# Performance work log

Hardware: AMD Instinct MI355X
Metric: run time of the kernel (lower is better)

The kernel has to match this reference:

```python
import jax, jax.numpy as jnp
import numpy as np

D_MODEL = 256
D_INNER = 512   # expand=2
D_STATE = 16
D_CONV = 4
DT_RANK = 16    # ceil(d_model/16)


def _mamba(x, in_w, conv_w, conv_b, xproj_w, dt_w, dt_b, A_log, Dskip, out_w):
    # x: (B, T, d_model)
    B, T, _ = x.shape
    xz = x @ in_w.T                       # (B, T, 2*d_inner)
    u, z = jnp.split(xz, 2, axis=-1)
    # depthwise causal conv1d over time
    uc = u.transpose(0, 2, 1)             # (B, d_inner, T)
    up = jnp.pad(uc, ((0, 0), (0, 0), (D_CONV - 1, 0)))
    conv = conv_b[None, :, None]
    for k in range(D_CONV):               # tiny fixed loop over taps
        conv = conv + conv_w[None, :, k, None] * up[:, :, k:k + T]
    u = jax.nn.silu(conv).transpose(0, 2, 1)   # (B, T, d_inner)
    # input-dependent SSM params
    x_dbl = u @ xproj_w.T                 # (B, T, dt_rank + 2*d_state)
    dt, Bm, Cm = jnp.split(x_dbl, [DT_RANK, DT_RANK + D_STATE], axis=-1)
    delta = jax.nn.softplus(dt @ dt_w.T + dt_b)   # (B, T, d_inner)
    A = -jnp.exp(A_log)                   # (d_inner, d_state)
    dA = jnp.exp(jnp.einsum('btd,dn->btdn', delta, A))
    dBu = jnp.einsum('btd,btn,btd->btdn', delta, Bm, u)

    def step(h, inp):
        dA_t, dBu_t, C_t = inp
        h = dA_t * h + dBu_t              # (B, d_inner, d_state)
        y = jnp.einsum('bdn,bn->bd', h, C_t)
        return h, y

    h0 = jnp.zeros((B, D_INNER, D_STATE), x.dtype)
    _, ys = jax.lax.scan(step, h0, (dA.transpose(1, 0, 2, 3),
                                    dBu.transpose(1, 0, 2, 3),
                                    Cm.transpose(1, 0, 2)))
    y = ys.transpose(1, 0, 2)             # (B, T, d_inner)
    y = y + u * Dskip
    y = y * jax.nn.silu(z)
    return y @ out_w.T                    # (B, T, d_model)


def _layernorm(x, w, b, eps=1e-5):
    mu = jnp.mean(x, axis=-1, keepdims=True)
    var = jnp.var(x, axis=-1, keepdims=True)
    return (x - mu) * jax.lax.rsqrt(var + eps) * w + b


def _mamba_params(key, scale=0.02):
    ks = jax.random.split(key, 6)
    A_log = jnp.log(jnp.broadcast_to(jnp.arange(1, D_STATE + 1, dtype=jnp.float32),
                                     (D_INNER, D_STATE)))
    return dict(
        in_w=jax.random.normal(ks[0], (2 * D_INNER, D_MODEL)) * scale,
        conv_w=jax.random.normal(ks[1], (D_INNER, D_CONV)) * scale,
        conv_b=jnp.zeros((D_INNER,)),
        xproj_w=jax.random.normal(ks[2], (DT_RANK + 2 * D_STATE, D_INNER)) * scale,
        dt_w=jax.random.normal(ks[3], (D_INNER, DT_RANK)) * scale,
        dt_b=jax.random.uniform(ks[4], (D_INNER,), minval=-4.0, maxval=-2.0),
        A_log=A_log,
        D=jnp.ones((D_INNER,)),
        out_w=jax.random.normal(ks[5], (D_MODEL, D_INNER)) * scale,
    )


def setup_inputs() -> dict:
    key = jax.random.key(0)
    kx, kf, kb, kfu = jax.random.split(key, 4)
    x = jax.random.normal(kx, (4, 2048, D_MODEL), dtype=jnp.float32)
    pf = _mamba_params(kf)
    pb = _mamba_params(kb)
    inp = {'x': x,
           'norm_w': jnp.ones((D_MODEL,)), 'norm_b': jnp.zeros((D_MODEL,)),
           'fus_w': jax.random.normal(kfu, (D_MODEL, 2 * D_MODEL)) * 0.02,
           'fus_b': jnp.zeros((D_MODEL,))}
    for k, v in pf.items():
        inp['f_' + k] = v
    for k, v in pb.items():
        inp['b_' + k] = v
    return inp


def reference(x, norm_w, norm_b, fus_w, fus_b,
              f_in_w, f_conv_w, f_conv_b, f_xproj_w, f_dt_w, f_dt_b, f_A_log, f_D, f_out_w,
              b_in_w, b_conv_w, b_conv_b, b_xproj_w, b_dt_w, b_dt_b, b_A_log, b_D, b_out_w):
    residual = x
    xn = _layernorm(x, norm_w, norm_b)
    x_fwd = _mamba(xn, f_in_w, f_conv_w, f_conv_b, f_xproj_w, f_dt_w, f_dt_b,
                   f_A_log, f_D, f_out_w)
    x_bwd = _mamba(jnp.flip(xn, axis=1), b_in_w, b_conv_w, b_conv_b, b_xproj_w,
                   b_dt_w, b_dt_b, b_A_log, b_D, b_out_w)
    x_bwd = jnp.flip(x_bwd, axis=1)
    x_cat = jnp.concatenate([x_fwd, x_bwd], axis=-1)
    out = x_cat @ fus_w.T + fus_b         # dropout is identity in eval mode
    return out + residual
```

## Files before the change

### kernel.cpp

```cpp
#include <hip/hip_runtime.h>
#include <hip/hip_fp16.h>
#include <math.h>

#define B_ 4
#define T_ 2048
#define DM 256
#define DI 512
#define DS 16
#define DR 16
#define M_ (B_*T_)
#define NCH 64
#define CLEN (T_/NCH)
#define XDS 64

typedef __attribute__((ext_vector_type(8))) short short8;
typedef __attribute__((ext_vector_type(4))) float f32x4;

__device__ __forceinline__ unsigned short f2bf(float f){
  unsigned u = __builtin_bit_cast(unsigned, f);
  u += 0x7fff + ((u >> 16) & 1);
  return (unsigned short)(u >> 16);
}
__device__ __forceinline__ float bf2f(unsigned short h){
  unsigned u = ((unsigned)h) << 16;
  return __builtin_bit_cast(float, u);
}
__device__ __forceinline__ unsigned short f2h(float f){
  __half h = __float2half(f);
  return __builtin_bit_cast(unsigned short, h);
}
__device__ __forceinline__ float h2f(unsigned short b){
  __half h = __builtin_bit_cast(__half, b);
  return __half2float(h);
}

__device__ __forceinline__ void pow_ladder(float r, float* a){
  a[0]=r; a[1]=r*r; a[2]=a[1]*r; a[3]=a[1]*a[1];
  a[4]=a[3]*r; a[5]=a[3]*a[1]; a[6]=a[3]*a[2]; a[7]=a[3]*a[3];
  a[8]=a[7]*a[0]; a[9]=a[7]*a[1]; a[10]=a[7]*a[2]; a[11]=a[7]*a[3];
  a[12]=a[7]*a[4]; a[13]=a[7]*a[5]; a[14]=a[7]*a[6]; a[15]=a[7]*a[7];
}

__device__ __forceinline__ void softplus_r(float x, float& dv, float& r){
  const float e = __expf(-fabsf(x));
  const float l = __logf(1.f + e);
  dv = fmaxf(x, 0.f) + l;
  r  = __fdividef(x > 0.f ? e : 1.f, 1.f + e);
}

__device__ __forceinline__ float wave_reduce_sum(float v){
  #pragma unroll
  for(int off=32; off; off>>=1) v += __shfl_xor(v, off, 64);
  return v;
}

__global__ __launch_bounds__(64)
void ln_kernel(const float* __restrict__ x, const float* __restrict__ w,
               const float* __restrict__ b, unsigned short* __restrict__ xnb){
  int row = blockIdx.x; int lane = threadIdx.x;
  const float4 v = *(const float4*)(x + (size_t)row*DM + lane*4);
  float s  = v.x+v.y+v.z+v.w;
  float sq = v.x*v.x+v.y*v.y+v.z*v.z+v.w*v.w;
  s = wave_reduce_sum(s); sq = wave_reduce_sum(sq);
  float mu  = s*(1.f/DM);
  float var = sq*(1.f/DM) - mu*mu;
  float rs  = rsqrtf(var + 1e-5f);
  const float4 wv = *(const float4*)(w + lane*4);
  const float4 bv = *(const float4*)(b + lane*4);
  ushort4 o;
  o.x = f2bf((v.x-mu)*rs*wv.x + bv.x);
  o.y = f2bf((v.y-mu)*rs*wv.y + bv.y);
  o.z = f2bf((v.z-mu)*rs*wv.z + bv.z);
  o.w = f2bf((v.w-mu)*rs*wv.w + bv.w);
  *(ushort4*)(xnb + (size_t)row*DM + lane*4) = o;
}

__global__ __launch_bounds__(256)
void wconv_kernel(const float* __restrict__ f_in_w, const float* __restrict__ b_in_w,
                  const float* __restrict__ f_out_w, const float* __restrict__ b_out_w,
                  const float* __restrict__ fus_w,
                  const float* __restrict__ f_xp, const float* __restrict__ b_xp,
                  unsigned short* __restrict__ dst){
  const int idx = blockIdx.x*256 + threadIdx.x;
  float v;
  if      (idx < 262144) v = f_in_w[idx];
  else if (idx < 524288) v = b_in_w[idx-262144];
  else if (idx < 655360) v = f_out_w[idx-524288];
  else if (idx < 786432) v = b_out_w[idx-655360];
  else if (idx < 917504) v = fus_w[idx-786432];
  else if (idx < 950272){ int j = idx-917504; v = (j < 48*512) ? f_xp[j] : 0.f; }
  else                  { int j = idx-950272; v = (j < 48*512) ? b_xp[j] : 0.f; }
  dst[idx] = f2bf(v);
}

#define GBM 128
#define GBN 64
#define GBK 32

template<typename OutT>
__global__ __launch_bounds__(256)
void gemm_mfma(const unsigned short* __restrict__ A, int lda, size_t sA,
               const unsigned short* __restrict__ W, int ldw, size_t sW,
               OutT* __restrict__ C, int ldc, size_t sC, int K,
               const float* __restrict__ bias,
               const float* __restrict__ resid, int ldr){
  A += (size_t)blockIdx.z * sA;
  W += (size_t)blockIdx.z * sW;
  C += (size_t)blockIdx.z * sC;
  __shared__ unsigned short smem[GBM*40 + GBN*40];
  unsigned short* As = smem;
  unsigned short* Ws = smem + GBM*40;
  const int tid = threadIdx.x;
  const int bm = blockIdx.y * GBM;
  const int bn = blockIdx.x * GBN;

  const int srow = tid >> 2;
  const int scol = (tid & 3) * 8;
  const unsigned short* Ag = A + (size_t)(bm + srow)*lda + scol;
  const unsigned short* Wg = W + (size_t)(bn + srow)*ldw + scol;

  const int wid = tid >> 6;
  const int lr  = tid & 15;
  const int lk  = ((tid >> 4) & 3) * 8;

  f32x4 acc[2][4];
  #pragma unroll
  for(int i=0;i<2;++i)
    #pragma unroll
    for(int j=0;j<4;++j) acc[i][j] = (f32x4){0.f,0.f,0.f,0.f};

  for(int k0=0; k0<K; k0+=GBK){
    const uint4 a0 = *(const uint4*)(Ag + k0);
    const uint4 a1 = *(const uint4*)(Ag + (size_t)64*lda + k0);
    const uint4 w0 = *(const uint4*)(Wg + k0);
    __syncthreads();
    *(uint4*)&As[srow*40 + scol]      = a0;
    *(uint4*)&As[(srow+64)*40 + scol] = a1;
    *(uint4*)&Ws[srow*40 + scol]      = w0;
    __syncthreads();

    const short8 af0 = *(const short8*)&As[(wid*32 + lr)*40 + lk];
    const short8 af1 = *(const short8*)&As[(wid*32 + 16 + lr)*40 + lk];
    #pragma unroll
    for(int nt=0; nt<4; ++nt){
      const short8 bfr = *(const short8*)&Ws[(nt*16 + lr)*40 + lk];
      acc[0][nt] = __builtin_amdgcn_mfma_f32_16x16x32_bf16(af0, bfr, acc[0][nt], 0, 0, 0);
      acc[1][nt] = __builtin_amdgcn_mfma_f32_16x16x32_bf16(af1, bfr, acc[1][nt], 0, 0, 0);
    }
  }

  const int rg = (tid >> 4) & 3;
  if constexpr (sizeof(OutT) == 2){
    unsigned short* rp = smem;
    #pragma unroll
    for(int half=0; half<2; ++half){
      __syncthreads();
      if((wid>>1) == half){
        const int lr0 = (wid & 1) * 32;
        #pragma unroll
        for(int mt=0; mt<2; ++mt)
          #pragma unroll
          for(int nt=0; nt<4; ++nt)
            #pragma unroll
            for(int r=0; r<4; ++r)
              rp[(lr0 + mt*16 + rg*4 + r)*72 + nt*16 + lr] = f2bf(acc[mt][nt][r]);
      }
      __syncthreads();
      #pragma unroll
      for(int rep=0; rep<2; ++rep){
        const int j = tid + rep*256;
        const int row = j >> 3, c8 = (j & 7) * 8;
        *(short8*)&C[(size_t)(bm + half*64 + row)*ldc + bn + c8] =
            *(const short8*)&rp[row*72 + c8];
      }
    }
  } else {
    #pragma unroll
    for(int mt=0; mt<2; ++mt){
      const int r0 = bm + wid*32 + mt*16 + rg*4;
      #pragma unroll
      for(int nt=0; nt<4; ++nt){
        const int c = bn + nt*16 + lr;
        #pragma unroll
        for(int r=0; r<4; ++r){
          float v = acc[mt][nt][r];
          if(bias)  v += bias[c];
          if(resid) v += resid[(size_t)(r0+r)*ldr + c];
          C[(size_t)(r0+r)*ldc + c] = v;
        }
      }
    }
  }
}

__device__ __forceinline__ void load_row8(const unsigned short* base, int t, float* dst){
  if(t >= 0 && t < T_){
    const short8 v = *(const short8*)(base + (size_t)t*1024);
    #pragma unroll
    for(int c=0;c<8;++c) dst[c] = bf2f((unsigned short)v[c]);
  } else {
    #pragma unroll
    for(int c=0;c<8;++c) dst[c] = 0.f;
  }
}

__global__ __launch_bounds__(256)
void conv_silu_kernel(const unsigned short* __restrict__ xz,
                      const float* __restrict__ fcw, const float* __restrict__ fcb,
                      const float* __restrict__ bcw, const float* __restrict__ bcb,
                      unsigned short* __restrict__ ub){
  const int dir = blockIdx.y;
  const int id  = blockIdx.x*256 + threadIdx.x;
  const int g   = id & 63;
  const int tt  = (id >> 6) & 255;
  const int b   = id >> 14;
  const int ch0 = g*8;
  const int t0  = tt*8;
  const float* cw = dir ? bcw : fcw;
  const float* cb = dir ? bcb : fcb;

  float kw0[8], kw1[8], kw2[8], kw3[8], bb[8];
  #pragma unroll
  for(int c=0;c<8;++c){
    const float4 w4 = *(const float4*)(cw + (ch0+c)*4);
    if(dir==0){ kw0[c]=w4.x; kw1[c]=w4.y; kw2[c]=w4.z; kw3[c]=w4.w; }
    else      { kw0[c]=w4.w; kw1[c]=w4.z; kw2[c]=w4.y; kw3[c]=w4.x; }
    bb[c] = cb[ch0+c];
  }

  const unsigned short* base = xz + (size_t)dir*M_*1024 + (size_t)b*T_*1024 + ch0;
  const int pre = dir ? 0 : -3;

  float w0[8], w1[8], w2[8];
  load_row8(base, t0+pre+0, w0);
  load_row8(base, t0+pre+1, w1);
  load_row8(base, t0+pre+2, w2);

  unsigned short* out = ub + (size_t)dir*M_*DI + ((size_t)b*T_+t0)*DI + ch0;
  #pragma unroll
  for(int i=0;i<8;++i){
    float cur[8];
    load_row8(base, t0+pre+3+i, cur);
    short8 o;
    #pragma unroll
    for(int c=0;c<8;++c){
      float a = bb[c];
      a = fmaf(kw0[c], w0[c], a);
      a = fmaf(kw1[c], w1[c], a);
      a = fmaf(kw2[c], w2[c], a);
      a = fmaf(kw3[c], cur[c], a);
      const float sg = 1.f/(1.f+__expf(-a));
      o[c] = (short)f2bf(a*sg);
    }
    *(short8*)(out + (size_t)i*DI) = o;
    #pragma unroll
    for(int c=0;c<8;++c){ w0[c]=w1[c]; w1[c]=w2[c]; w2[c]=cur[c]; }
  }
}


__global__ __launch_bounds__(256)
void scanA_kernel(const unsigned short* __restrict__ u, const float* __restrict__ xdbl,
                  const float* __restrict__ fdw, const float* __restrict__ fdb,
                  const float* __restrict__ bdw, const float* __restrict__ bdb,
                  const float* __restrict__ fD, const float* __restrict__ bD,
                  float* __restrict__ Sdvb, float* __restrict__ qb,
                  unsigned int* __restrict__ ye){
  __shared__ float sX[CLEN][48];
  const int tid  = threadIdx.x;
  const int bx   = blockIdx.x;
  const int dir  = bx >> 3;
  const int b    = (bx >> 1) & 3;
  const int half = bx & 1;
  const int chunk= blockIdx.y;
  const int d    = half*256 + tid;
  const int i0   = chunk*CLEN;

  #pragma unroll
  for(int rep=0; rep<2; ++rep){
    const int j = tid + rep*256;
    if(j < CLEN*12){
      const int r = j / 12, c4 = (j % 12) * 4;
      const int t = dir ? (T_-1-(i0+r)) : (i0+r);
      const float4 v = *(const float4*)(xdbl + (size_t)dir*M_*XDS + ((size_t)b*T_+t)*XDS + c4);
      *(float4*)&sX[r][c4] = v;
    }
  }

  float wr[16];
  {
    const float* wsrc = (dir ? bdw : fdw) + d*DR;
    #pragma unroll
    for(int g=0; g<4; ++g){
      const float4 v = *(const float4*)(wsrc + g*4);
      wr[g*4]=v.x; wr[g*4+1]=v.y; wr[g*4+2]=v.z; wr[g*4+3]=v.w;
    }
  }
  const float dtb = (dir ? bdb : fdb)[d];
  const float Dd  = (dir ? bD : fD)[d];
  __syncthreads();

  const int t0 = dir ? (T_-1-i0) : i0;
  const ptrdiff_t sst = dir ? -DI : DI;
  const unsigned short* up = u + (size_t)dir*M_*DI + ((size_t)b*T_+t0)*DI + d;
  unsigned int* yep = ye + (size_t)dir*M_*DI + ((size_t)b*T_+t0)*DI + d;

  float h[16];
  #pragma unroll
  for(int n=0;n<16;++n) h[n]=0.f;
  float Sdv = 0.f, ecum = 1.f;

  unsigned short uvr = *up;
  for(int i=0; i<CLEN; ++i){
    up += sst;
    const unsigned short uvn = *up;
    float4 t0v = *(const float4*)&sX[i][0];
    float4 t1v = *(const float4*)&sX[i][4];
    float4 t2v = *(const float4*)&sX[i][8];
    float4 t3v = *(const float4*)&sX[i][12];
    float x = dtb;
    x = fmaf(t0v.x,wr[0], fmaf(t0v.y,wr[1], fmaf(t0v.z,wr[2], fmaf(t0v.w,wr[3], x))));
    x = fmaf(t1v.x,wr[4], fmaf(t1v.y,wr[5], fmaf(t1v.z,wr[6], fmaf(t1v.w,wr[7], x))));
    x = fmaf(t2v.x,wr[8], fmaf(t2v.y,wr[9], fmaf(t2v.z,wr[10],fmaf(t2v.w,wr[11],x))));
    x = fmaf(t3v.x,wr[12],fmaf(t3v.y,wr[13],fmaf(t3v.z,wr[14],fmaf(t3v.w,wr[15],x))));
    float dv, r_;
    softplus_r(x, dv, r_);
    Sdv += dv;
    ecum *= r_;
    const float uv = bf2f(uvr);
    const float du = dv*uv;
    float a[16];
    pow_ladder(r_, a);
    float4 b0 = *(const float4*)&sX[i][16];
    float4 b1 = *(const float4*)&sX[i][20];
    float4 b2 = *(const float4*)&sX[i][24];
    float4 b3 = *(const float4*)&sX[i][28];
    float4 c0 = *(const float4*)&sX[i][32];
    float4 c1 = *(const float4*)&sX[i][36];
    float4 c2 = *(const float4*)&sX[i][40];
    float4 c3 = *(const float4*)&sX[i][44];
    const float bl[16] = {b0.x,b0.y,b0.z,b0.w, b1.x,b1.y,b1.z,b1.w,
                          b2.x,b2.y,b2.z,b2.w, b3.x,b3.y,b3.z,b3.w};
    const float cl[16] = {c0.x,c0.y,c0.z,c0.w, c1.x,c1.y,c1.z,c1.w,
                          c2.x,c2.y,c2.z,c2.w, c3.x,c3.y,c3.z,c3.w};
    float y0=0.f, y1=0.f, y2=0.f, y3=0.f;
    #pragma unroll
    for(int n=0;n<16;n+=4){
      h[n+0] = fmaf(a[n+0], h[n+0], du*bl[n+0]);
      h[n+1] = fmaf(a[n+1], h[n+1], du*bl[n+1]);
      h[n+2] = fmaf(a[n+2], h[n+2], du*bl[n+2]);
      h[n+3] = fmaf(a[n+3], h[n+3], du*bl[n+3]);
      y0 = fmaf(h[n+0], cl[n+0], y0);
      y1 = fmaf(h[n+1], cl[n+1], y1);
      y2 = fmaf(h[n+2], cl[n+2], y2);
      y3 = fmaf(h[n+3], cl[n+3], y3);
    }
    const float ylocal = ((y0+y1)+(y2+y3)) + uv*Dd;
    const unsigned int pe = (unsigned int)(unsigned short)(ecum*65535.f + 0.5f);
    *yep = ((unsigned int)f2h(ylocal)) | (pe << 16);
    yep += sst;
    uvr = uvn;
  }

  const int cidx = (dir*4+b)*512 + d;
  Sdvb[(size_t)chunk*4096 + cidx] = Sdv;
  float* qp = qb + (size_t)chunk*65536 + ((size_t)cidx<<4);
  #pragma unroll
  for(int g=0; g<4; ++g)
    *(float4*)(qp + g*4) = make_float4(h[g*4],h[g*4+1],h[g*4+2],h[g*4+3]);
}

__global__ __launch_bounds__(256)
void scanB_kernel(const float* __restrict__ Sdvb, const float* __restrict__ qb,
                  float* __restrict__ hs){
  const int id = blockIdx.x*256 + threadIdx.x;
  const int c  = id >> 4;
  const float np1 = -(float)((id & 15) + 1);
  float h = 0.f;
  for(int ch=0; ch<NCH; ++ch){
    const size_t idx = (size_t)ch*65536 + id;
    hs[idx] = h;
    const float P = __expf(np1 * Sdvb[(size_t)ch*4096 + c]);
    h = fmaf(P, h, qb[idx]);
  }
}

__global__ __launch_bounds__(256)
void scanC_kernel(const unsigned int* __restrict__ ye, const float* __restrict__ xdbl,
                  const unsigned short* __restrict__ xz,
                  const float* __restrict__ hs, unsigned short* __restrict__ yb){
  __shared__ float sC[CLEN][16];
  const int tid  = threadIdx.x;
  const int bx   = blockIdx.x;
  const int dir  = bx >> 3;
  const int b    = (bx >> 1) & 3;
  const int half = bx & 1;
  const int chunk= blockIdx.y;
  const int d    = half*256 + tid;
  const int i0   = chunk*CLEN;

  if(tid < CLEN*4){
    const int r = tid >> 2, c4 = (tid & 3) * 4;
    const int t = dir ? (T_-1-(i0+r)) : (i0+r);
    const float4 v = *(const float4*)(xdbl + (size_t)dir*M_*XDS + ((size_t)b*T_+t)*XDS + 32 + c4);
    *(float4*)&sC[r][c4] = v;
  }

  const int cidx = (dir*4+b)*512 + d;
  float g[16];
  {
    const float* hp = hs + (size_t)chunk*65536 + ((size_t)cidx<<4);
    #pragma unroll
    for(int q=0; q<4; ++q){
      float4 v = *(const float4*)(hp + q*4);
      g[q*4]=v.x; g[q*4+1]=v.y; g[q*4+2]=v.z; g[q*4+3]=v.w;
    }
  }
  __syncthreads();

  const int t0 = dir ? (T_-1-i0) : i0;
  const ptrdiff_t sst = dir ? -DI : DI;
  const ptrdiff_t zst = dir ? -1024 : 1024;
  const unsigned int*  yep = ye + (size_t)dir*M_*DI + ((size_t)b*T_+t0)*DI + d;
  const unsigned short* zp = xz + (size_t)dir*M_*1024 + ((size_t)b*T_+t0)*1024 + 512 + d;
  unsigned short* yp = yb + (size_t)dir*M_*DI + ((size_t)b*T_+t0)*DI + d;

  unsigned int pk = *yep; unsigned short zv = *zp;
  for(int i=0; i<CLEN; ++i){
    yep += sst; zp += zst;
    const unsigned int pkn = *yep; const unsigned short zvn = *zp;
    const float ylocal = h2f((unsigned short)(pk & 0xffff));
    const float e = (float)(pk >> 16) * (1.f/65535.f);
    float w[16];
    pow_ladder(e, w);
    const float4 c0 = *(const float4*)&sC[i][0];
    const float4 c1 = *(const float4*)&sC[i][4];
    const float4 c2 = *(const float4*)&sC[i][8];
    const float4 c3 = *(const float4*)&sC[i][12];
    const float cl[16] = {c0.x,c0.y,c0.z,c0.w, c1.x,c1.y,c1.z,c1.w,
                          c2.x,c2.y,c2.z,c2.w, c3.x,c3.y,c3.z,c3.w};
    float s0=0.f, s1=0.f, s2=0.f, s3=0.f;
    #pragma unroll
    for(int n=0;n<16;n+=4){
      s0 = fmaf(cl[n+0]*g[n+0], w[n+0], s0);
      s1 = fmaf(cl[n+1]*g[n+1], w[n+1], s1);
      s2 = fmaf(cl[n+2]*g[n+2], w[n+2], s2);
      s3 = fmaf(cl[n+3]*g[n+3], w[n+3], s3);
    }
    const float y = ylocal + ((s0+s1)+(s2+s3));
    const float zf = bf2f(zv);
    const float sg = __fdividef(zf, 1.f + __expf(-zf));
    *yp = f2bf(y * sg);
    yp += sst;
    pk = pkn; zv = zvn;
  }
}

extern "C" void kernel_launch(void* const* d_in, const int* in_sizes, int n_in,
                              void* d_out, int out_size, void* d_ws, size_t ws_size,
                              hipStream_t stream) {
  const float* x       = (const float*)d_in[0];
  const float* norm_w  = (const float*)d_in[1];
  const float* norm_b  = (const float*)d_in[2];
  const float* fus_w   = (const float*)d_in[3];
  const float* fus_b   = (const float*)d_in[4];
  const float* f_in_w  = (const float*)d_in[5];
  const float* f_conv_w= (const float*)d_in[6];
  const float* f_conv_b= (const float*)d_in[7];
  const float* f_xproj = (const float*)d_in[8];
  const float* f_dt_w  = (const float*)d_in[9];
  const float* f_dt_b  = (const float*)d_in[10];
  const float* f_A_log = (const float*)d_in[11];
  const float* f_D     = (const float*)d_in[12];
  const float* f_out_w = (const float*)d_in[13];
  const float* b_in_w  = (const float*)d_in[14];
  const float* b_conv_w= (const float*)d_in[15];
  const float* b_conv_b= (const float*)d_in[16];
  const float* b_xproj = (const float*)d_in[17];
  const float* b_dt_w  = (const float*)d_in[18];
  const float* b_dt_b  = (const float*)d_in[19];
  const float* b_A_log = (const float*)d_in[20];
  const float* b_D     = (const float*)d_in[21];
  const float* b_out_w = (const float*)d_in[22];
  (void)f_A_log; (void)b_A_log;

  float* xdbl  = (float*)d_ws;
  float* qb    = xdbl + (size_t)2*M_*XDS;
  float* hsb   = qb   + (size_t)NCH*65536;
  float* Sdvb  = hsb  + (size_t)NCH*65536;
  unsigned int* ye = (unsigned int*)(Sdvb + (size_t)NCH*4096);
  unsigned short* xz_bf  = (unsigned short*)(ye + (size_t)2*M_*DI);
  unsigned short* xn_bf  = xz_bf  + (size_t)2*M_*1024;
  unsigned short* u_bf   = xn_bf  + (size_t)M_*DM;
  unsigned short* y_bf   = u_bf   + (size_t)2*M_*DI;
  unsigned short* xcat_bf= y_bf   + (size_t)2*M_*DI;
  unsigned short* w_bf   = xcat_bf+ (size_t)M_*DI;
  unsigned short* wf_in  = w_bf;
  unsigned short* wf_out = w_bf + 524288;
  unsigned short* wfus   = w_bf + 786432;
  unsigned short* wf_xp  = w_bf + 917504;

  wconv_kernel<<<3840, 256, 0, stream>>>(f_in_w, b_in_w, f_out_w, b_out_w,
                                         fus_w, f_xproj, b_xproj, w_bf);

  ln_kernel<<<M_, 64, 0, stream>>>(x, norm_w, norm_b, xn_bf);

  gemm_mfma<unsigned short><<<dim3(1024/GBN, M_/GBM, 2), 256, 0, stream>>>(
      xn_bf, DM, 0, wf_in, DM, 262144, xz_bf, 1024, (size_t)M_*1024, DM,
      nullptr, nullptr, 0);

  conv_silu_kernel<<<dim3(256, 2), 256, 0, stream>>>(
      xz_bf, f_conv_w, f_conv_b, b_conv_w, b_conv_b, u_bf);

  gemm_mfma<float><<<dim3(1, M_/GBM, 2), 256, 0, stream>>>(
      u_bf, DI, (size_t)M_*DI, wf_xp, DI, 32768, xdbl, XDS, (size_t)M_*XDS, DI,
      nullptr, nullptr, 0);

  scanA_kernel<<<dim3(16, NCH), 256, 0, stream>>>(u_bf, xdbl, f_dt_w, f_dt_b,
                                                  b_dt_w, b_dt_b, f_D, b_D,
                                                  Sdvb, qb, ye);
  scanB_kernel<<<256, 256, 0, stream>>>(Sdvb, qb, hsb);
  scanC_kernel<<<dim3(16, NCH), 256, 0, stream>>>(ye, xdbl, xz_bf, hsb, y_bf);

  gemm_mfma<unsigned short><<<dim3(256/GBN, M_/GBM, 2), 256, 0, stream>>>(
      y_bf, DI, (size_t)M_*DI, wf_out, DI, 131072, xcat_bf, 512, 256, DI,
      nullptr, nullptr, 0);

  gemm_mfma<float><<<dim3(256/GBN, M_/GBM, 1), 256, 0, stream>>>(
      xcat_bf, DI, 0, wfus, DI, 0, (float*)d_out, 256, 0, DI, fus_b, x, DM);
}
```

Measured before the change: 171.2 us.

## Fuse three scan phases into one cooperative kernel with grid syncs

Merges the chunked scan's local pass, inter-chunk carry pass and correction pass into a single cooperative kernel separated by grid-wide barriers. The packed per-step local outputs stay in shared memory (32KB per block) instead of a global round trip, and the C coefficients staged in shared memory are reused. This removes two launches and a large global buffer write and read. In exchange, all 1024 blocks must be co-resident for the grid syncs, which limits occupancy, and the carry phase uses only 256 blocks while the rest wait.

Result: slower. 418.1 us (+144.3%).

```diff
diff --git a/kernel.cpp b/kernel.cpp
--- a/kernel.cpp
+++ b/kernel.cpp
@@ -1,6 +1,9 @@
 #include <hip/hip_runtime.h>
 #include <hip/hip_fp16.h>
+#include <hip/hip_cooperative_groups.h>
 #include <math.h>
+
+namespace cg = cooperative_groups;
 
 #define B_ 4
 #define T_ 2048
@@ -259,20 +262,23 @@
 }
 
 
-__global__ __launch_bounds__(256)
-void scanA_kernel(const unsigned short* __restrict__ u, const float* __restrict__ xdbl,
-                  const float* __restrict__ fdw, const float* __restrict__ fdb,
-                  const float* __restrict__ bdw, const float* __restrict__ bdb,
-                  const float* __restrict__ fD, const float* __restrict__ bD,
-                  float* __restrict__ Sdvb, float* __restrict__ qb,
-                  unsigned int* __restrict__ ye){
+__global__ __launch_bounds__(256, 4)
+void scan_fused(const unsigned short* __restrict__ u, const float* __restrict__ xdbl,
+                const unsigned short* __restrict__ xz,
+                const float* __restrict__ fdw, const float* __restrict__ fdb,
+                const float* __restrict__ bdw, const float* __restrict__ bdb,
+                const float* __restrict__ fD, const float* __restrict__ bD,
+                float* __restrict__ Sdvb, float* __restrict__ qb,
+                float* __restrict__ hsb, unsigned short* __restrict__ yb){
   __shared__ float sX[CLEN][48];
+  __shared__ unsigned int pkLds[CLEN*256];
   const int tid  = threadIdx.x;
-  const int bx   = blockIdx.x;
+  const int bid  = blockIdx.x;
+  const int bx   = bid & 15;
+  const int chunk= bid >> 4;
   const int dir  = bx >> 3;
   const int b    = (bx >> 1) & 3;
   const int half = bx & 1;
-  const int chunk= blockIdx.y;
   const int d    = half*256 + tid;
   const int i0   = chunk*CLEN;
 
@@ -303,156 +309,134 @@
   const int t0 = dir ? (T_-1-i0) : i0;
   const ptrdiff_t sst = dir ? -DI : DI;
   const unsigned short* up = u + (size_t)dir*M_*DI + ((size_t)b*T_+t0)*DI + d;
-  unsigned int* yep = ye + (size_t)dir*M_*DI + ((size_t)b*T_+t0)*DI + d;
-
-  float h[16];
-  #pragma unroll
-  for(int n=0;n<16;++n) h[n]=0.f;
-  float Sdv = 0.f, ecum = 1.f;
-
-  unsigned short uvr = *up;
-  for(int i=0; i<CLEN; ++i){
-    up += sst;
-    const unsigned short uvn = *up;
-    float4 t0v = *(const float4*)&sX[i][0];
-    float4 t1v = *(const float4*)&sX[i][4];
-    float4 t2v = *(const float4*)&sX[i][8];
-    float4 t3v = *(const float4*)&sX[i][12];
-    float x = dtb;
-    x = fmaf(t0v.x,wr[0], fmaf(t0v.y,wr[1], fmaf(t0v.z,wr[2], fmaf(t0v.w,wr[3], x))));
-    x = fmaf(t1v.x,wr[4], fmaf(t1v.y,wr[5], fmaf(t1v.z,wr[6], fmaf(t1v.w,wr[7], x))));
-    x = fmaf(t2v.x,wr[8], fmaf(t2v.y,wr[9], fmaf(t2v.z,wr[10],fmaf(t2v.w,wr[11],x))));
-    x = fmaf(t3v.x,wr[12],fmaf(t3v.y,wr[13],fmaf(t3v.z,wr[14],fmaf(t3v.w,wr[15],x))));
-    float dv, r_;
-    softplus_r(x, dv, r_);
-    Sdv += dv;
-    ecum *= r_;
-    const float uv = bf2f(uvr);
-    const float du = dv*uv;
-    float a[16];
-    pow_ladder(r_, a);
-    float4 b0 = *(const float4*)&sX[i][16];
-    float4 b1 = *(const float4*)&sX[i][20];
-    float4 b2 = *(const float4*)&sX[i][24];
-    float4 b3 = *(const float4*)&sX[i][28];
-    float4 c0 = *(const float4*)&sX[i][32];
-    float4 c1 = *(const float4*)&sX[i][36];
-    float4 c2 = *(const float4*)&sX[i][40];
-    float4 c3 = *(const float4*)&sX[i][44];
-    const float bl[16] = {b0.x,b0.y,b0.z,b0.w, b1.x,b1.y,b1.z,b1.w,
-                          b2.x,b2.y,b2.z,b2.w, b3.x,b3.y,b3.z,b3.w};
-    const float cl[16] = {c0.x,c0.y,c0.z,c0.w, c1.x,c1.y,c1.z,c1.w,
-                          c2.x,c2.y,c2.z,c2.w, c3.x,c3.y,c3.z,c3.w};
-    float y0=0.f, y1=0.f, y2=0.f, y3=0.f;
-    #pragma unroll
-    for(int n=0;n<16;n+=4){
-      h[n+0] = fmaf(a[n+0], h[n+0], du*bl[n+0]);
-      h[n+1] = fmaf(a[n+1], h[n+1], du*bl[n+1]);
-      h[n+2] = fmaf(a[n+2], h[n+2], du*bl[n+2]);
-      h[n+3] = fmaf(a[n+3], h[n+3], du*bl[n+3]);
-      y0 = fmaf(h[n+0], cl[n+0], y0);
-      y1 = fmaf(h[n+1], cl[n+1], y1);
-      y2 = fmaf(h[n+2], cl[n+2], y2);
-      y3 = fmaf(h[n+3], cl[n+3], y3);
-    }
-    const float ylocal = ((y0+y1)+(y2+y3)) + uv*Dd;
-    const unsigned int pe = (unsigned int)(unsigned short)(ecum*65535.f + 0.5f);
-    *yep = ((unsigned int)f2h(ylocal)) | (pe << 16);
-    yep += sst;
-    uvr = uvn;
-  }
-
-  const int cidx = (dir*4+b)*512 + d;
-  Sdvb[(size_t)chunk*4096 + cidx] = Sdv;
-  float* qp = qb + (size_t)chunk*65536 + ((size_t)cidx<<4);
-  #pragma unroll
-  for(int g=0; g<4; ++g)
-    *(float4*)(qp + g*4) = make_float4(h[g*4],h[g*4+1],h[g*4+2],h[g*4+3]);
-}
-
-__global__ __launch_bounds__(256)
-void scanB_kernel(const float* __restrict__ Sdvb, const float* __restrict__ qb,
-                  float* __restrict__ hs){
-  const int id = blockIdx.x*256 + threadIdx.x;
-  const int c  = id >> 4;
-  const float np1 = -(float)((id & 15) + 1);
-  float h = 0.f;
-  for(int ch=0; ch<NCH; ++ch){
-    const size_t idx = (size_t)ch*65536 + id;
-    hs[idx] = h;
-    const float P = __expf(np1 * Sdvb[(size_t)ch*4096 + c]);
-    h = fmaf(P, h, qb[idx]);
-  }
-}
-
-__global__ __launch_bounds__(256)
-void scanC_kernel(const unsigned int* __restrict__ ye, const float* __restrict__ xdbl,
-                  const unsigned short* __restrict__ xz,
-                  const float* __restrict__ hs, unsigned short* __restrict__ yb){
-  __shared__ float sC[CLEN][16];
-  const int tid  = threadIdx.x;
-  const int bx   = blockIdx.x;
-  const int dir  = bx >> 3;
-  const int b    = (bx >> 1) & 3;
-  const int half = bx & 1;
-  const int chunk= blockIdx.y;
-  const int d    = half*256 + tid;
-  const int i0   = chunk*CLEN;
-
-  if(tid < CLEN*4){
-    const int r = tid >> 2, c4 = (tid & 3) * 4;
-    const int t = dir ? (T_-1-(i0+r)) : (i0+r);
-    const float4 v = *(const float4*)(xdbl + (size_t)dir*M_*XDS + ((size_t)b*T_+t)*XDS + 32 + c4);
-    *(float4*)&sC[r][c4] = v;
-  }
-
-  const int cidx = (dir*4+b)*512 + d;
-  float g[16];
+
   {
-    const float* hp = hs + (size_t)chunk*65536 + ((size_t)cidx<<4);
-    #pragma unroll
-    for(int q=0; q<4; ++q){
-      float4 v = *(const float4*)(hp + q*4);
-      g[q*4]=v.x; g[q*4+1]=v.y; g[q*4+2]=v.z; g[q*4+3]=v.w;
-    }
-  }
-  __syncthreads();
-
-  const int t0 = dir ? (T_-1-i0) : i0;
-  const ptrdiff_t sst = dir ? -DI : DI;
-  const ptrdiff_t zst = dir ? -1024 : 1024;
-  const unsigned int*  yep = ye + (size_t)dir*M_*DI + ((size_t)b*T_+t0)*DI + d;
-  const unsigned short* zp = xz + (size_t)dir*M_*1024 + ((size_t)b*T_+t0)*1024 + 512 + d;
-  unsigned short* yp = yb + (size_t)dir*M_*DI + ((size_t)b*T_+t0)*DI + d;
-
-  unsigned int pk = *yep; unsigned short zv = *zp;
-  for(int i=0; i<CLEN; ++i){
-    yep += sst; zp += zst;
-    const unsigned int pkn = *yep; const unsigned short zvn = *zp;
-    const float ylocal = h2f((unsigned short)(pk & 0xffff));
-    const float e = (float)(pk >> 16) * (1.f/65535.f);
-    float w[16];
-    pow_ladder(e, w);
-    const float4 c0 = *(const float4*)&sC[i][0];
-    const float4 c1 = *(const float4*)&sC[i][4];
-    const float4 c2 = *(const float4*)&sC[i][8];
-    const float4 c3 = *(const float4*)&sC[i][12];
-    const float cl[16] = {c0.x,c0.y,c0.z,c0.w, c1.x,c1.y,c1.z,c1.w,
-                          c2.x,c2.y,c2.z,c2.w, c3.x,c3.y,c3.z,c3.w};
-    float s0=0.f, s1=0.f, s2=0.f, s3=0.f;
-    #pragma unroll
-    for(int n=0;n<16;n+=4){
-      s0 = fmaf(cl[n+0]*g[n+0], w[n+0], s0);
-      s1 = fmaf(cl[n+1]*g[n+1], w[n+1], s1);
-      s2 = fmaf(cl[n+2]*g[n+2], w[n+2], s2);
-      s3 = fmaf(cl[n+3]*g[n+3], w[n+3], s3);
-    }
-    const float y = ylocal + ((s0+s1)+(s2+s3));
-    const float zf = bf2f(zv);
-    const float sg = __fdividef(zf, 1.f + __expf(-zf));
-    *yp = f2bf(y * sg);
-    yp += sst;
-    pk = pkn; zv = zvn;
+    float h[16];
+    #pragma unroll
+    for(int n=0;n<16;++n) h[n]=0.f;
+    float Sdv = 0.f, ecum = 1.f;
+
+    unsigned short uvr = *up;
+    for(int i=0; i<CLEN; ++i){
+      up += sst;
+      const unsigned short uvn = *up;
+      float4 t0v = *(const float4*)&sX[i][0];
+      float4 t1v = *(const float4*)&sX[i][4];
+      float4 t2v = *(const float4*)&sX[i][8];
+      float4 t3v = *(const float4*)&sX[i][12];
+      float x = dtb;
+      x = fmaf(t0v.x,wr[0], fmaf(t0v.y,wr[1], fmaf(t0v.z,wr[2], fmaf(t0v.w,wr[3], x))));
+      x = fmaf(t1v.x,wr[4], fmaf(t1v.y,wr[5], fmaf(t1v.z,wr[6], fmaf(t1v.w,wr[7], x))));
+      x = fmaf(t2v.x,wr[8], fmaf(t2v.y,wr[9], fmaf(t2v.z,wr[10],fmaf(t2v.w,wr[11],x))));
+      x = fmaf(t3v.x,wr[12],fmaf(t3v.y,wr[13],fmaf(t3v.z,wr[14],fmaf(t3v.w,wr[15],x))));
+      float dv, r_;
+      softplus_r(x, dv, r_);
+      Sdv += dv;
+      ecum *= r_;
+      const float uv = bf2f(uvr);
+      const float du = dv*uv;
+      float a[16];
+      pow_ladder(r_, a);
+      float4 b0 = *(const float4*)&sX[i][16];
+      float4 b1 = *(const float4*)&sX[i][20];
+      float4 b2 = *(const float4*)&sX[i][24];
+      float4 b3 = *(const float4*)&sX[i][28];
+      float4 c0 = *(const float4*)&sX[i][32];
+      float4 c1 = *(const float4*)&sX[i][36];
+      float4 c2 = *(const float4*)&sX[i][40];
+      float4 c3 = *(const float4*)&sX[i][44];
+      const float bl[16] = {b0.x,b0.y,b0.z,b0.w, b1.x,b1.y,b1.z,b1.w,
+                            b2.x,b2.y,b2.z,b2.w, b3.x,b3.y,b3.z,b3.w};
+      const float cl[16] = {c0.x,c0.y,c0.z,c0.w, c1.x,c1.y,c1.z,c1.w,
+                            c2.x,c2.y,c2.z,c2.w, c3.x,c3.y,c3.z,c3.w};
+      float y0=0.f, y1=0.f, y2=0.f, y3=0.f;
+      #pragma unroll
+      for(int n=0;n<16;n+=4){
+        h[n+0] = fmaf(a[n+0], h[n+0], du*bl[n+0]);
+        h[n+1] = fmaf(a[n+1], h[n+1], du*bl[n+1]);
+        h[n+2] = fmaf(a[n+2], h[n+2], du*bl[n+2]);
+        h[n+3] = fmaf(a[n+3], h[n+3], du*bl[n+3]);
+        y0 = fmaf(h[n+0], cl[n+0], y0);
+        y1 = fmaf(h[n+1], cl[n+1], y1);
+        y2 = fmaf(h[n+2], cl[n+2], y2);
+        y3 = fmaf(h[n+3], cl[n+3], y3);
+      }
+      const float ylocal = ((y0+y1)+(y2+y3)) + uv*Dd;
+      const unsigned int pe = (unsigned int)(unsigned short)(ecum*65535.f + 0.5f);
+      pkLds[i*256 + tid] = ((unsigned int)f2h(ylocal)) | (pe << 16);
+      uvr = uvn;
+    }
+
+    const int cidx = (dir*4+b)*512 + d;
+    Sdvb[(size_t)chunk*4096 + cidx] = Sdv;
+    float* qp = qb + (size_t)chunk*65536 + ((size_t)cidx<<4);
+    #pragma unroll
+    for(int g=0; g<4; ++g)
+      *(float4*)(qp + g*4) = make_float4(h[g*4],h[g*4+1],h[g*4+2],h[g*4+3]);
+  }
+
+  cg::this_grid().sync();
+
+  if(bid < 256){
+    const int id = bid*256 + tid;
+    const int c  = id >> 4;
+    const float np1 = -(float)((id & 15) + 1);
+    float h = 0.f;
+    for(int ch=0; ch<NCH; ++ch){
+      const size_t idx = (size_t)ch*65536 + id;
+      hsb[idx] = h;
+      const float P = __expf(np1 * Sdvb[(size_t)ch*4096 + c]);
+      h = fmaf(P, h, qb[idx]);
+    }
+  }
+
+  cg::this_grid().sync();
+
+  {
+    const int cidx = (dir*4+b)*512 + d;
+    float g[16];
+    {
+      const float* hp = hsb + (size_t)chunk*65536 + ((size_t)cidx<<4);
+      #pragma unroll
+      for(int q=0; q<4; ++q){
+        float4 v = *(const float4*)(hp + q*4);
+        g[q*4]=v.x; g[q*4+1]=v.y; g[q*4+2]=v.z; g[q*4+3]=v.w;
+      }
+    }
+    const ptrdiff_t zst = dir ? -1024 : 1024;
+    const unsigned short* zp = xz + (size_t)dir*M_*1024 + ((size_t)b*T_+t0)*1024 + 512 + d;
+    unsigned short* yp = yb + (size_t)dir*M_*DI + ((size_t)b*T_+t0)*DI + d;
+
+    unsigned short zv = *zp;
+    for(int i=0; i<CLEN; ++i){
+      zp += zst;
+      const unsigned short zvn = *zp;
+      const unsigned int pk = pkLds[i*256 + tid];
+      const float ylocal = h2f((unsigned short)(pk & 0xffff));
+      const float e = (float)(pk >> 16) * (1.f/65535.f);
+      float w[16];
+      pow_ladder(e, w);
+      const float4 c0 = *(const float4*)&sX[i][32];
+      const float4 c1 = *(const float4*)&sX[i][36];
+      const float4 c2 = *(const float4*)&sX[i][40];
+      const float4 c3 = *(const float4*)&sX[i][44];
+      const float cl[16] = {c0.x,c0.y,c0.z,c0.w, c1.x,c1.y,c1.z,c1.w,
+                            c2.x,c2.y,c2.z,c2.w, c3.x,c3.y,c3.z,c3.w};
+      float s0=0.f, s1=0.f, s2=0.f, s3=0.f;
+      #pragma unroll
+      for(int n=0;n<16;n+=4){
+        s0 = fmaf(cl[n+0]*g[n+0], w[n+0], s0);
+        s1 = fmaf(cl[n+1]*g[n+1], w[n+1], s1);
+        s2 = fmaf(cl[n+2]*g[n+2], w[n+2], s2);
+        s3 = fmaf(cl[n+3]*g[n+3], w[n+3], s3);
+      }
+      const float y = ylocal + ((s0+s1)+(s2+s3));
+      const float zf = bf2f(zv);
+      const float sg = __fdividef(zf, 1.f + __expf(-zf));
+      *yp = f2bf(y * sg);
+      yp += sst;
+      zv = zvn;
+    }
   }
 }
 
@@ -488,8 +472,7 @@
   float* qb    = xdbl + (size_t)2*M_*XDS;
   float* hsb   = qb   + (size_t)NCH*65536;
   float* Sdvb  = hsb  + (size_t)NCH*65536;
-  unsigned int* ye = (unsigned int*)(Sdvb + (size_t)NCH*4096);
-  unsigned short* xz_bf  = (unsigned short*)(ye + (size_t)2*M_*DI);
+  unsigned short* xz_bf  = (unsigned short*)(Sdvb + (size_t)NCH*4096);
   unsigned short* xn_bf  = xz_bf  + (size_t)2*M_*1024;
   unsigned short* u_bf   = xn_bf  + (size_t)M_*DM;
   unsigned short* y_bf   = u_bf   + (size_t)2*M_*DI;
@@ -516,11 +499,14 @@
       u_bf, DI, (size_t)M_*DI, wf_xp, DI, 32768, xdbl, XDS, (size_t)M_*XDS, DI,
       nullptr, nullptr, 0);
 
-  scanA_kernel<<<dim3(16, NCH), 256, 0, stream>>>(u_bf, xdbl, f_dt_w, f_dt_b,
-                                                  b_dt_w, b_dt_b, f_D, b_D,
-                                                  Sdvb, qb, ye);
-  scanB_kernel<<<256, 256, 0, stream>>>(Sdvb, qb, hsb);
-  scanC_kernel<<<dim3(16, NCH), 256, 0, stream>>>(ye, xdbl, xz_bf, hsb, y_bf);
+  {
+    void* args[] = {(void*)&u_bf, (void*)&xdbl, (void*)&xz_bf,
+                    (void*)&f_dt_w, (void*)&f_dt_b, (void*)&b_dt_w, (void*)&b_dt_b,
+                    (void*)&f_D, (void*)&b_D,
+                    (void*)&Sdvb, (void*)&qb, (void*)&hsb, (void*)&y_bf};
+    hipLaunchCooperativeKernel((void*)scan_fused, dim3(16*NCH), dim3(256),
+                               args, 0, stream);
+  }
 
   gemm_mfma<unsigned short><<<dim3(256/GBN, M_/GBM, 2), 256, 0, stream>>>(
       y_bf, DI, (size_t)M_*DI, wf_out, DI, 131072, xcat_bf, 512, 256, DI,
```

## Fold out_proj weights into fusion weights and merge two GEMMs

Applied to the files above, without the earlier changes.

Precomputes a combined weight matrix by multiplying the fusion weight halves with the transposed out_proj weights. scanC now writes both directions into one concatenated buffer, and a single K=1024 GEMM replaces the out_proj and fusion GEMMs. This removes an intermediate buffer round trip and halves the GEMM FLOPs. In exchange it adds a small transpose and a weight GEMM every call, plus an extra bf16 rounding of the combined weights.

Measured after the change: 173.5 us. Within noise of the previous version (+1.3%).

```diff
diff --git a/kernel.cpp b/kernel.cpp
--- a/kernel.cpp
+++ b/kernel.cpp
@@ -91,6 +91,15 @@
   else if (idx < 950272){ int j = idx-917504; v = (j < 48*512) ? f_xp[j] : 0.f; }
   else                  { int j = idx-950272; v = (j < 48*512) ? b_xp[j] : 0.f; }
   dst[idx] = f2bf(v);
+}
+
+__global__ __launch_bounds__(256)
+void wtrans_kernel(const unsigned short* __restrict__ w_out_bf,
+                   unsigned short* __restrict__ outT){
+  const int dir = blockIdx.y;
+  const int j   = blockIdx.x;
+  const int k   = threadIdx.x;
+  outT[(size_t)dir*131072 + j*256 + k] = w_out_bf[(size_t)dir*131072 + k*512 + j];
 }
 
 #define GBM 128
@@ -388,7 +397,7 @@
 __global__ __launch_bounds__(256)
 void scanC_kernel(const unsigned int* __restrict__ ye, const float* __restrict__ xdbl,
                   const unsigned short* __restrict__ xz,
-                  const float* __restrict__ hs, unsigned short* __restrict__ yb){
+                  const float* __restrict__ hs, unsigned short* __restrict__ ycat){
   __shared__ float sC[CLEN][16];
   const int tid  = threadIdx.x;
   const int bx   = blockIdx.x;
@@ -421,9 +430,10 @@
   const int t0 = dir ? (T_-1-i0) : i0;
   const ptrdiff_t sst = dir ? -DI : DI;
   const ptrdiff_t zst = dir ? -1024 : 1024;
+  const ptrdiff_t yst = dir ? -1024 : 1024;
   const unsigned int*  yep = ye + (size_t)dir*M_*DI + ((size_t)b*T_+t0)*DI + d;
   const unsigned short* zp = xz + (size_t)dir*M_*1024 + ((size_t)b*T_+t0)*1024 + 512 + d;
-  unsigned short* yp = yb + (size_t)dir*M_*DI + ((size_t)b*T_+t0)*DI + d;
+  unsigned short* yp = ycat + ((size_t)b*T_+t0)*1024 + dir*512 + d;
 
   unsigned int pk = *yep; unsigned short zv = *zp;
   for(int i=0; i<CLEN; ++i){
@@ -451,7 +461,7 @@
     const float zf = bf2f(zv);
     const float sg = __fdividef(zf, 1.f + __expf(-zf));
     *yp = f2bf(y * sg);
-    yp += sst;
+    yp += yst;
     pk = pkn; zv = zvn;
   }
 }
@@ -492,16 +502,23 @@
   unsigned short* xz_bf  = (unsigned short*)(ye + (size_t)2*M_*DI);
   unsigned short* xn_bf  = xz_bf  + (size_t)2*M_*1024;
   unsigned short* u_bf   = xn_bf  + (size_t)M_*DM;
-  unsigned short* y_bf   = u_bf   + (size_t)2*M_*DI;
-  unsigned short* xcat_bf= y_bf   + (size_t)2*M_*DI;
-  unsigned short* w_bf   = xcat_bf+ (size_t)M_*DI;
+  unsigned short* ycat_bf= u_bf   + (size_t)2*M_*DI;
+  unsigned short* w_bf   = ycat_bf+ (size_t)M_*1024;
   unsigned short* wf_in  = w_bf;
   unsigned short* wf_out = w_bf + 524288;
   unsigned short* wfus   = w_bf + 786432;
   unsigned short* wf_xp  = w_bf + 917504;
+  unsigned short* outT   = w_bf + 983040;
+  unsigned short* Wcat   = outT + 262144;
 
   wconv_kernel<<<3840, 256, 0, stream>>>(f_in_w, b_in_w, f_out_w, b_out_w,
                                          fus_w, f_xproj, b_xproj, w_bf);
+
+  wtrans_kernel<<<dim3(512, 2), 256, 0, stream>>>(wf_out, outT);
+
+  gemm_mfma<unsigned short><<<dim3(512/GBN, 256/GBM, 2), 256, 0, stream>>>(
+      wfus, 512, 256, outT, 256, 131072, Wcat, 1024, 512, 256,
+      nullptr, nullptr, 0);
 
   ln_kernel<<<M_, 64, 0, stream>>>(x, norm_w, norm_b, xn_bf);
 
@@ -520,12 +537,9 @@
                                                   b_dt_w, b_dt_b, f_D, b_D,
                                                   Sdvb, qb, ye);
   scanB_kernel<<<256, 256, 0, stream>>>(Sdvb, qb, hsb);
-  scanC_kernel<<<dim3(16, NCH), 256, 0, stream>>>(ye, xdbl, xz_bf, hsb, y_bf);
-
-  gemm_mfma<unsigned short><<<dim3(256/GBN, M_/GBM, 2), 256, 0, stream>>>(
-      y_bf, DI, (size_t)M_*DI, wf_out, DI, 131072, xcat_bf, 512, 256, DI,
-      nullptr, nullptr, 0);
+  scanC_kernel<<<dim3(16, NCH), 256, 0, stream>>>(ye, xdbl, xz_bf, hsb, ycat_bf);
 
   gemm_mfma<float><<<dim3(256/GBN, M_/GBM, 1), 256, 0, stream>>>(
-      xcat_bf, DI, 0, wfus, DI, 0, (float*)d_out, 256, 0, DI, fus_b, x, DM);
-}
+      ycat_bf, 1024, 0, Wcat, 1024, 0, (float*)d_out, 256, 0, 1024,
+      fus_b, x, DM);
+}
```
